# Kernel optimization log

Hardware: AMD Instinct MI355X
Metric: run time of the kernel (lower is better)

Reference implementation:

```python
import jax, jax.numpy as jnp
import numpy as np

D = 4096
N = 8192


def fwht(x):
    """Fast Walsh-Hadamard Transform (orthonormal, divided by sqrt(d)).

    log2(d) butterfly stages, each a single vectorized add/sub over the
    full tensor. Loop bound is static (log2 of trailing dim), jit-safe.
    """
    d = x.shape[-1]
    leading = x.shape[:-1]
    h = 1
    while h < d:
        x = x.reshape(*leading, d // (2 * h), 2, h)
        a = x[..., 0, :]
        b = x[..., 1, :]
        x = jnp.stack([a + b, a - b], axis=-2).reshape(*leading, d)
        h *= 2
    return x * jnp.asarray(d, x.dtype) ** -0.5


def setup_inputs() -> dict:
    key = jax.random.key(0)
    kx, ks = jax.random.split(key)
    x = jax.random.normal(kx, (N, D), dtype=jnp.float32)
    # deterministic random +/-1 sign vector (buffer of RHTRotation)
    signs = (jax.random.randint(ks, (D,), 0, 2).astype(jnp.float32) * 2.0 - 1.0)
    return {"x": x, "signs": signs}


def reference(x, signs):
    # randomized_hadamard: y = H @ (D x) / sqrt(d), D = diag(signs)
    return fwht(x * signs)
```

## Files before the change

kernel.cpp:

```cpp
#include <hip/hip_runtime.h>

#define D 4096

__device__ __forceinline__ void fwht16(float v[16]) {
#pragma unroll
    for (int s = 1; s < 16; s <<= 1) {
#pragma unroll
        for (int i = 0; i < 16; i++) {
            if (!(i & s)) {
                float a = v[i], b = v[i ^ s];
                v[i]     = a + b;
                v[i ^ s] = a - b;
            }
        }
    }
}

__global__ __launch_bounds__(256) void fwht_kernel(const float* __restrict__ x,
                                                   const float* __restrict__ signs,
                                                   float* __restrict__ out) {
    __shared__ float lds[4352];

    const int t = threadIdx.x;
    const long row = blockIdx.x;
    const float* __restrict__ xr = x + row * (long)D;
    float* __restrict__ orow = out + row * (long)D;

    float v[16];

    {
        const float4* __restrict__ xv = (const float4*)(xr + t * 16);
        const float4* __restrict__ sv = (const float4*)(signs + t * 16);
#pragma unroll
        for (int k = 0; k < 4; k++) {
            float4 a = xv[k];
            float4 s = sv[k];
            v[4 * k + 0] = a.x * s.x;
            v[4 * k + 1] = a.y * s.y;
            v[4 * k + 2] = a.z * s.z;
            v[4 * k + 3] = a.w * s.w;
        }
    }
    fwht16(v);

#pragma unroll
    for (int b = 0; b < 16; b++) lds[17 * t + b] = v[b];
    __syncthreads();

    {
        const int a2 = t >> 4, b = t & 15;
        const int base = a2 * 272 + b;
#pragma unroll
        for (int a1 = 0; a1 < 16; a1++) v[a1] = lds[base + a1 * 17];
        fwht16(v);
#pragma unroll
        for (int a1 = 0; a1 < 16; a1++) lds[base + a1 * 17] = v[a1];
    }
    __syncthreads();

    {
        const int base = (t >> 4) * 17 + (t & 15);
#pragma unroll
        for (int a2 = 0; a2 < 16; a2++) v[a2] = lds[base + a2 * 272];
        fwht16(v);
        const float scale = 1.0f / 64.0f;
#pragma unroll
        for (int a2 = 0; a2 < 16; a2++) orow[a2 * 256 + t] = v[a2] * scale;
    }
}

extern "C" void kernel_launch(void* const* d_in, const int* in_sizes, int n_in,
                              void* d_out, int out_size, void* d_ws, size_t ws_size,
                              hipStream_t stream) {
    const float* x = (const float*)d_in[0];
    const float* signs = (const float*)d_in[1];
    float* out = (float*)d_out;
    const int rows = in_sizes[0] / D;
    fwht_kernel<<<dim3(rows), dim3(256), 0, stream>>>(x, signs, out);
}
```

Measured before the change: 226.4 us.

## Process four rows per block with next-row prefetch and coalesced index mapping

Each block now transforms four consecutive rows. The global load of the next row is issued while the current row goes through its LDS transpose stages. The per-thread element mapping is changed so that global loads and stores are fully coalesced float4 or float accesses, and the final output index is remapped to match. The sign vector is loaded once per block instead of once per row, and the launch bound requests higher occupancy. In exchange there is extra register pressure from the prefetch buffer, fewer blocks overall, and an extra barrier per row to protect LDS reuse.

```diff
diff --git a/kernel.cpp b/kernel.cpp
--- a/kernel.cpp
+++ b/kernel.cpp
@@ -1,6 +1,7 @@
 #include <hip/hip_runtime.h>
 
 #define D 4096
+#define RPB 4
 
 __device__ __forceinline__ void fwht16(float v[16]) {
 #pragma unroll
@@ -16,56 +17,91 @@
     }
 }
 
-__global__ __launch_bounds__(256) void fwht_kernel(const float* __restrict__ x,
-                                                   const float* __restrict__ signs,
-                                                   float* __restrict__ out) {
+__device__ __forceinline__ void lds_barrier() {
+    asm volatile("s_waitcnt lgkmcnt(0)" ::: "memory");
+    __builtin_amdgcn_s_barrier();
+}
+
+__global__ __launch_bounds__(256, 6) void fwht_kernel(const float* __restrict__ x,
+                                                      const float* __restrict__ signs,
+                                                      float* __restrict__ out) {
     __shared__ float lds[4352];
 
     const int t = threadIdx.x;
-    const long row = blockIdx.x;
-    const float* __restrict__ xr = x + row * (long)D;
-    float* __restrict__ orow = out + row * (long)D;
+    const long row0 = (long)blockIdx.x * RPB;
 
-    float v[16];
+    float s[16];
+    {
+        const float4* __restrict__ sv = (const float4*)signs;
+#pragma unroll
+        for (int k = 0; k < 4; k++) {
+            float4 g = sv[k * 256 + t];
+            s[4 * k + 0] = g.x; s[4 * k + 1] = g.y;
+            s[4 * k + 2] = g.z; s[4 * k + 3] = g.w;
+        }
+    }
+
+    float v[16], u[16];
 
     {
-        const float4* __restrict__ xv = (const float4*)(xr + t * 16);
-        const float4* __restrict__ sv = (const float4*)(signs + t * 16);
+        const float4* __restrict__ xv = (const float4*)(x + row0 * (long)D);
 #pragma unroll
         for (int k = 0; k < 4; k++) {
-            float4 a = xv[k];
-            float4 s = sv[k];
-            v[4 * k + 0] = a.x * s.x;
-            v[4 * k + 1] = a.y * s.y;
-            v[4 * k + 2] = a.z * s.z;
-            v[4 * k + 3] = a.w * s.w;
+            float4 a = xv[k * 256 + t];
+            v[4 * k + 0] = a.x * s[4 * k + 0];
+            v[4 * k + 1] = a.y * s[4 * k + 1];
+            v[4 * k + 2] = a.z * s[4 * k + 2];
+            v[4 * k + 3] = a.w * s[4 * k + 3];
         }
     }
-    fwht16(v);
+
+    const int a2    = t >> 4, bb = t & 15;
+    const int base2 = a2 * 272 + bb;
+    const int p3    = (t >> 2) & 15;
+    const int base3 = 17 * p3 + ((t >> 6) << 2) + (t & 3);
+    const int outoff = (t >> 6) * 1024 + (t & 63);
+
+    for (int i = 0; i < RPB; i++) {
+        fwht16(v);
+#pragma unroll
+        for (int q = 0; q < 16; q++) lds[17 * t + q] = v[q];
+
+        if (i + 1 < RPB) {
+            const float4* __restrict__ xv =
+                (const float4*)(x + (row0 + i + 1) * (long)D);
+#pragma unroll
+            for (int k = 0; k < 4; k++) {
+                float4 a = xv[k * 256 + t];
+                u[4 * k + 0] = a.x; u[4 * k + 1] = a.y;
+                u[4 * k + 2] = a.z; u[4 * k + 3] = a.w;
+            }
+        }
+
+        lds_barrier();
 
 #pragma unroll
-    for (int b = 0; b < 16; b++) lds[17 * t + b] = v[b];
-    __syncthreads();
-
-    {
-        const int a2 = t >> 4, b = t & 15;
-        const int base = a2 * 272 + b;
-#pragma unroll
-        for (int a1 = 0; a1 < 16; a1++) v[a1] = lds[base + a1 * 17];
+        for (int a1 = 0; a1 < 16; a1++) v[a1] = lds[base2 + a1 * 17];
         fwht16(v);
 #pragma unroll
-        for (int a1 = 0; a1 < 16; a1++) lds[base + a1 * 17] = v[a1];
-    }
-    __syncthreads();
+        for (int a1 = 0; a1 < 16; a1++) lds[base2 + a1 * 17] = v[a1];
 
-    {
-        const int base = (t >> 4) * 17 + (t & 15);
+        lds_barrier();
+
 #pragma unroll
-        for (int a2 = 0; a2 < 16; a2++) v[a2] = lds[base + a2 * 272];
+        for (int c = 0; c < 16; c++) v[c] = lds[base3 + c * 272];
         fwht16(v);
-        const float scale = 1.0f / 64.0f;
+        {
+            const float scale = 1.0f / 64.0f;
+            float* __restrict__ orow = out + (row0 + i) * (long)D + outoff;
 #pragma unroll
-        for (int a2 = 0; a2 < 16; a2++) orow[a2 * 256 + t] = v[a2] * scale;
+            for (int c = 0; c < 16; c++) orow[c * 64] = v[c] * scale;
+        }
+
+        if (i + 1 < RPB) {
+            __builtin_amdgcn_s_barrier();
+#pragma unroll
+            for (int q = 0; q < 16; q++) v[q] = u[q] * s[q];
+        }
     }
 }
 
@@ -76,5 +112,5 @@
     const float* signs = (const float*)d_in[1];
     float* out = (float*)d_out;
     const int rows = in_sizes[0] / D;
-    fwht_kernel<<<dim3(rows), dim3(256), 0, stream>>>(x, signs, out);
+    fwht_kernel<<<dim3(rows / RPB), dim3(256), 0, stream>>>(x, signs, out);
 }
```

Result: slower. 236.2 us (+4.3%).

## Coalesce float4 loads with strided element mapping and use nontemporal stores

Applied to the files above, without the earlier changes.

Each thread now loads its float4 chunks strided across the row (k*256+t), so a wavefront reads contiguous memory per instruction instead of each thread reading 64 contiguous bytes. The index mapping through LDS is reworked to match, using a padded layout (stride 17 plus a 273 group stride) to avoid bank conflicts. Output is written with nontemporal stores to avoid polluting the cache. The element permutation is more complex and the final store pattern is scattered in 4-byte granules, which may cost some write coalescing.

```diff
diff --git a/kernel.cpp b/kernel.cpp
--- a/kernel.cpp
+++ b/kernel.cpp
@@ -19,22 +19,20 @@
 __global__ __launch_bounds__(256) void fwht_kernel(const float* __restrict__ x,
                                                    const float* __restrict__ signs,
                                                    float* __restrict__ out) {
-    __shared__ float lds[4352];
+    __shared__ float lds[4368];
 
     const int t = threadIdx.x;
     const long row = blockIdx.x;
-    const float* __restrict__ xr = x + row * (long)D;
-    float* __restrict__ orow = out + row * (long)D;
 
     float v[16];
 
     {
-        const float4* __restrict__ xv = (const float4*)(xr + t * 16);
-        const float4* __restrict__ sv = (const float4*)(signs + t * 16);
+        const float4* __restrict__ xv = (const float4*)(x + row * (long)D);
+        const float4* __restrict__ sv = (const float4*)signs;
 #pragma unroll
         for (int k = 0; k < 4; k++) {
-            float4 a = xv[k];
-            float4 s = sv[k];
+            float4 a = xv[k * 256 + t];
+            float4 s = sv[k * 256 + t];
             v[4 * k + 0] = a.x * s.x;
             v[4 * k + 1] = a.y * s.y;
             v[4 * k + 2] = a.z * s.z;
@@ -43,29 +41,35 @@
     }
     fwht16(v);
 
+    {
+        const int wbase = 17 * t + (t >> 4);
 #pragma unroll
-    for (int b = 0; b < 16; b++) lds[17 * t + b] = v[b];
-    __syncthreads();
-
-    {
-        const int a2 = t >> 4, b = t & 15;
-        const int base = a2 * 272 + b;
-#pragma unroll
-        for (int a1 = 0; a1 < 16; a1++) v[a1] = lds[base + a1 * 17];
-        fwht16(v);
-#pragma unroll
-        for (int a1 = 0; a1 < 16; a1++) lds[base + a1 * 17] = v[a1];
+        for (int q = 0; q < 16; q++) lds[wbase + q] = v[q];
     }
     __syncthreads();
 
     {
-        const int base = (t >> 4) * 17 + (t & 15);
+        const int base = 273 * (t >> 4) + (t & 15);
 #pragma unroll
-        for (int a2 = 0; a2 < 16; a2++) v[a2] = lds[base + a2 * 272];
+        for (int B = 0; B < 16; B++) v[B] = lds[base + 17 * B];
         fwht16(v);
+#pragma unroll
+        for (int B = 0; B < 16; B++) lds[base + 17 * B] = v[B];
+    }
+    __syncthreads();
+
+    {
+        const int base = 17 * (t & 15) + (t >> 4);
+        float u[16];
+#pragma unroll
+        for (int A = 0; A < 16; A++) u[A] = lds[base + 273 * A];
+        fwht16(u);
         const float scale = 1.0f / 64.0f;
+        float* __restrict__ orow = out + row * (long)D
+                                 + ((t >> 6) * 1024) + ((t & 15) * 4) + ((t >> 4) & 3);
 #pragma unroll
-        for (int a2 = 0; a2 < 16; a2++) orow[a2 * 256 + t] = v[a2] * scale;
+        for (int A = 0; A < 16; A++)
+            __builtin_nontemporal_store(u[A] * scale, orow + A * 64);
     }
 }
 
```

New measurement: 228.8 us. About the same (+1.1%).

## Use single-wavefront 64x64 radix FWHT with XOR-swizzled LDS transpose

Applied to the files above, without the earlier changes.

Restructures each row's 4096-point transform from three radix-16 passes across 256 threads into two radix-64 passes done by one 64-lane wavefront, each lane holding 64 values in registers. The transpose between passes goes through LDS with an XOR swizzle to avoid bank conflicts. Because the block is a single wave, the code drops __syncthreads and uses only an LDS waitcnt plus a sched barrier. This removes a barrier and an LDS round-trip. In exchange each lane needs far more registers, which may lower occupancy, and the input loads are strided 256 bytes per lane, so they are less coalesced.

```diff
diff --git a/kernel.cpp b/kernel.cpp
--- a/kernel.cpp
+++ b/kernel.cpp
@@ -2,11 +2,11 @@
 
 #define D 4096
 
-__device__ __forceinline__ void fwht16(float v[16]) {
+__device__ __forceinline__ void fwht64(float v[64]) {
 #pragma unroll
-    for (int s = 1; s < 16; s <<= 1) {
+    for (int s = 1; s < 64; s <<= 1) {
 #pragma unroll
-        for (int i = 0; i < 16; i++) {
+        for (int i = 0; i < 64; i++) {
             if (!(i & s)) {
                 float a = v[i], b = v[i ^ s];
                 v[i]     = a + b;
@@ -16,23 +16,21 @@
     }
 }
 
-__global__ __launch_bounds__(256) void fwht_kernel(const float* __restrict__ x,
-                                                   const float* __restrict__ signs,
-                                                   float* __restrict__ out) {
-    __shared__ float lds[4352];
+__global__ __launch_bounds__(64) void fwht_kernel(const float* __restrict__ x,
+                                                  const float* __restrict__ signs,
+                                                  float* __restrict__ out) {
+    __shared__ float lds[4096];
 
-    const int t = threadIdx.x;
+    const int l = threadIdx.x;
     const long row = blockIdx.x;
-    const float* __restrict__ xr = x + row * (long)D;
-    float* __restrict__ orow = out + row * (long)D;
 
-    float v[16];
+    float v[64];
 
     {
-        const float4* __restrict__ xv = (const float4*)(xr + t * 16);
-        const float4* __restrict__ sv = (const float4*)(signs + t * 16);
+        const float4* __restrict__ xv = (const float4*)(x + row * (long)D + l * 64);
+        const float4* __restrict__ sv = (const float4*)(signs + l * 64);
 #pragma unroll
-        for (int k = 0; k < 4; k++) {
+        for (int k = 0; k < 16; k++) {
             float4 a = xv[k];
             float4 s = sv[k];
             v[4 * k + 0] = a.x * s.x;
@@ -41,32 +39,21 @@
             v[4 * k + 3] = a.w * s.w;
         }
     }
-    fwht16(v);
+    fwht64(v);
 
 #pragma unroll
-    for (int b = 0; b < 16; b++) lds[17 * t + b] = v[b];
-    __syncthreads();
+    for (int r = 0; r < 64; r++) lds[64 * r + (l ^ r)] = v[r];
+    asm volatile("s_waitcnt lgkmcnt(0)" ::: "memory");
+    __builtin_amdgcn_sched_barrier(0);
+#pragma unroll
+    for (int r = 0; r < 64; r++) v[r] = lds[64 * l + (l ^ r)];
 
-    {
-        const int a2 = t >> 4, b = t & 15;
-        const int base = a2 * 272 + b;
+    fwht64(v);
+
+    const float scale = 1.0f / 64.0f;
+    float* __restrict__ orow = out + row * (long)D + l;
 #pragma unroll
-        for (int a1 = 0; a1 < 16; a1++) v[a1] = lds[base + a1 * 17];
-        fwht16(v);
-#pragma unroll
-        for (int a1 = 0; a1 < 16; a1++) lds[base + a1 * 17] = v[a1];
-    }
-    __syncthreads();
-
-    {
-        const int base = (t >> 4) * 17 + (t & 15);
-#pragma unroll
-        for (int a2 = 0; a2 < 16; a2++) v[a2] = lds[base + a2 * 272];
-        fwht16(v);
-        const float scale = 1.0f / 64.0f;
-#pragma unroll
-        for (int a2 = 0; a2 < 16; a2++) orow[a2 * 256 + t] = v[a2] * scale;
-    }
+    for (int r = 0; r < 64; r++) orow[64 * r] = v[r] * scale;
 }
 
 extern "C" void kernel_launch(void* const* d_in, const int* in_sizes, int n_in,
@@ -76,5 +63,5 @@
     const float* signs = (const float*)d_in[1];
     float* out = (float*)d_out;
     const int rows = in_sizes[0] / D;
-    fwht_kernel<<<dim3(rows), dim3(256), 0, stream>>>(x, signs, out);
+    fwht_kernel<<<dim3(rows), dim3(64), 0, stream>>>(x, signs, out);
 }
```

Measured after the change: 245.1 us. 8.3% more time.
